# Performance work log

Measured on AMD Instinct MI355X. Metric: run time of the kernel, lower is better.

Reference implementation:

```python
import jax, jax.numpy as jnp
import numpy as np


def setup_inputs() -> dict:
    key = jax.random.key(0)
    B, C, H, W = 64, 128, 64, 64
    x = jax.random.normal(key, (B, C, H, W), dtype=jnp.float32)
    return {"x": x}


def reference(x) -> jnp.ndarray:
    # Covariance pooling: y = x_flat @ I_hat @ x_flat^T with
    # I_hat = (1/M) I - (1/M^2) ones(M,M).
    # Algebraically identical to (1/M) * (x - mean)(x - mean)^T, which
    # avoids materializing the MxM centering matrix.
    B, C, H, W = x.shape
    M = H * W
    xf = x.reshape(B, C, M)
    xc = xf - jnp.mean(xf, axis=2, keepdims=True)  # center over spatial dim
    y = jnp.einsum('bcm,bdm->bcd', xc, xc) / M     # [B, C, C]
    return y
```

## Files before the change

kernel.cpp:

```cpp
#include <hip/hip_runtime.h>
#include <hip/hip_bf16.h>

typedef __bf16 bf16x8 __attribute__((ext_vector_type(8)));
typedef float  f32x4  __attribute__((ext_vector_type(4)));

#define B_      64
#define C_      128
#define M_      4096
#define KCHUNK  4
#define KC      (M_ / KCHUNK)
#define BK      64
#define NSLAB   (KC / BK)
#define LSTR    72

__device__ __forceinline__ unsigned short f2bf(float f) {
  unsigned u = __builtin_bit_cast(unsigned, f);
  u += 0x7fffu + ((u >> 16) & 1u);
  return (unsigned short)(u >> 16);
}

__global__ __launch_bounds__(256) void covpool_main(
    const float* __restrict__ x, float* __restrict__ Gp, float* __restrict__ Sp) {
  __shared__ unsigned short As[2][C_ * LSTR];

  const int tid = threadIdx.x;
  const int b   = blockIdx.x >> 2;
  const int ch  = blockIdx.x & 3;

  const int r  = tid >> 2;
  const int c4 = (tid & 3) << 4;

  const float* xp0 = x + ((size_t)(b * C_ + r) * M_) + (size_t)ch * KC + c4;
  const float* xp1 = xp0 + (size_t)64 * M_;

  const int lane = tid & 63;
  const int wave = tid >> 6;
  const int row0 = (wave >> 1) << 6;
  const int col0 = (wave & 1) << 6;
  const int lrow = lane & 15;
  const int quad = lane >> 4;

  f32x4 acc[4][4];
#pragma unroll
  for (int i = 0; i < 4; ++i)
#pragma unroll
    for (int j = 0; j < 4; ++j)
      acc[i][j] = (f32x4){0.f, 0.f, 0.f, 0.f};

  float sum0 = 0.f, sum1 = 0.f;

  float4 regs[2][8];
#pragma unroll
  for (int q = 0; q < 4; ++q) {
    regs[0][q]     = ((const float4*)xp0)[q];
    regs[0][4 + q] = ((const float4*)xp1)[q];
  }

  for (int s = 0; s < NSLAB; ++s) {
    const int cur = s & 1;
    if (s + 1 < NSLAB) {
      const float4* p0 = (const float4*)(xp0 + (size_t)(s + 1) * BK);
      const float4* p1 = (const float4*)(xp1 + (size_t)(s + 1) * BK);
#pragma unroll
      for (int q = 0; q < 4; ++q) {
        regs[cur ^ 1][q]     = p0[q];
        regs[cur ^ 1][4 + q] = p1[q];
      }
    }
    unsigned short* d0 = &As[cur][r * LSTR + c4];
    unsigned short* d1 = &As[cur][(64 + r) * LSTR + c4];
#pragma unroll
    for (int q = 0; q < 4; ++q) {
      float4 v = regs[cur][q];
      sum0 += (v.x + v.y) + (v.z + v.w);
      ushort4 pk0 = { f2bf(v.x), f2bf(v.y), f2bf(v.z), f2bf(v.w) };
      *(ushort4*)(d0 + q * 4) = pk0;
      float4 w = regs[cur][4 + q];
      sum1 += (w.x + w.y) + (w.z + w.w);
      ushort4 pk1 = { f2bf(w.x), f2bf(w.y), f2bf(w.z), f2bf(w.w) };
      *(ushort4*)(d1 + q * 4) = pk1;
    }
    __syncthreads();

#pragma unroll
    for (int ks = 0; ks < 2; ++ks) {
      const int koff = ks * 32 + quad * 8;
      bf16x8 af[4], bfr[4];
#pragma unroll
      for (int i = 0; i < 4; ++i)
        af[i] = *(const bf16x8*)&As[cur][(row0 + i * 16 + lrow) * LSTR + koff];
#pragma unroll
      for (int j = 0; j < 4; ++j)
        bfr[j] = *(const bf16x8*)&As[cur][(col0 + j * 16 + lrow) * LSTR + koff];
#pragma unroll
      for (int i = 0; i < 4; ++i)
#pragma unroll
        for (int j = 0; j < 4; ++j)
          acc[i][j] = __builtin_amdgcn_mfma_f32_16x16x32_bf16(af[i], bfr[j], acc[i][j], 0, 0, 0);
    }
    __syncthreads();
  }

  float* gout = Gp + (((size_t)ch * B_ + b) << 14);
#pragma unroll
  for (int i = 0; i < 4; ++i)
#pragma unroll
    for (int j = 0; j < 4; ++j)
#pragma unroll
      for (int rr = 0; rr < 4; ++rr)
        gout[(size_t)(row0 + i * 16 + quad * 4 + rr) * C_ + (col0 + j * 16 + lrow)] = acc[i][j][rr];

  sum0 += __shfl_xor(sum0, 1); sum0 += __shfl_xor(sum0, 2);
  sum1 += __shfl_xor(sum1, 1); sum1 += __shfl_xor(sum1, 2);
  if ((tid & 3) == 0) {
    float* sout = Sp + (((size_t)ch * B_ + b) << 7);
    sout[r]      = sum0;
    sout[64 + r] = sum1;
  }
}

__global__ __launch_bounds__(256) void covpool_fix(
    const float* __restrict__ Gp, const float* __restrict__ Sp, float* __restrict__ y) {
  const int idx = blockIdx.x * 256 + threadIdx.x;
  const int bb  = idx >> 14;
  const int rem = idx & 16383;
  const int cc  = rem >> 7;
  const int dd  = rem & 127;
  float g = 0.f, sc = 0.f, sd = 0.f;
#pragma unroll
  for (int ch = 0; ch < KCHUNK; ++ch) {
    g  += Gp[(((size_t)ch * B_ + bb) << 14) + rem];
    sc += Sp[(((size_t)ch * B_ + bb) << 7) + cc];
    sd += Sp[(((size_t)ch * B_ + bb) << 7) + dd];
  }
  const float invM = 1.f / (float)M_;
  y[idx] = g * invM - (sc * invM) * (sd * invM);
}

extern "C" void kernel_launch(void* const* d_in, const int* in_sizes, int n_in,
                              void* d_out, int out_size, void* d_ws, size_t ws_size,
                              hipStream_t stream) {
  const float* x = (const float*)d_in[0];
  float* out = (float*)d_out;
  float* wsG = (float*)d_ws;
  float* wsS = wsG + (size_t)KCHUNK * B_ * C_ * C_;
  covpool_main<<<dim3(B_ * KCHUNK), dim3(256), 0, stream>>>(x, wsG, wsS);
  covpool_fix<<<dim3((B_ * C_ * C_) / 256), dim3(256), 0, stream>>>(wsG, wsS, out);
}
```

Before: 229.8 us.

## Split K into 8 chunks, use 512-thread blocks, store bf16 partial Gram matrices

Doubles the K split so 512 blocks cover the GPU instead of 256. Blocks grow to 512 threads (8 waves, each computing a 64x32 tile), and the slab loop is manually unrolled into an explicit double buffer. Partial Gram sums are written as bf16 to halve workspace traffic, and the reduction kernel is vectorized to handle four outputs per thread. Rounding the partials to bf16 adds precision error on top of the bf16 inputs, which could threaten tolerance, especially after the mean subtraction.

Result: faster. 195.9 us (-14.7%).

```diff
diff --git a/kernel.cpp b/kernel.cpp
--- a/kernel.cpp
+++ b/kernel.cpp
@@ -1,13 +1,13 @@
 #include <hip/hip_runtime.h>
-#include <hip/hip_bf16.h>
 
 typedef __bf16 bf16x8 __attribute__((ext_vector_type(8)));
 typedef float  f32x4  __attribute__((ext_vector_type(4)));
+typedef unsigned short us8 __attribute__((ext_vector_type(8)));
 
 #define B_      64
 #define C_      128
 #define M_      4096
-#define KCHUNK  4
+#define KCHUNK  8
 #define KC      (M_ / KCHUNK)
 #define BK      64
 #define NSLAB   (KC / BK)
@@ -18,123 +18,143 @@
   u += 0x7fffu + ((u >> 16) & 1u);
   return (unsigned short)(u >> 16);
 }
+__device__ __forceinline__ float bf2f(unsigned short h) {
+  unsigned u = ((unsigned)h) << 16;
+  return __builtin_bit_cast(float, u);
+}
 
-__global__ __launch_bounds__(256) void covpool_main(
-    const float* __restrict__ x, float* __restrict__ Gp, float* __restrict__ Sp) {
+__global__ __launch_bounds__(512, 4) void covpool_main(
+    const float* __restrict__ x, unsigned short* __restrict__ Gp, float* __restrict__ Sp) {
   __shared__ unsigned short As[2][C_ * LSTR];
 
-  const int tid = threadIdx.x;
-  const int b   = blockIdx.x >> 2;
-  const int ch  = blockIdx.x & 3;
+  const int tid  = threadIdx.x;
+  const int b    = blockIdx.x >> 3;
+  const int ch   = blockIdx.x & 7;
 
-  const int r  = tid >> 2;
-  const int c4 = (tid & 3) << 4;
+  const int row  = tid >> 3;
+  const int col8 = tid & 7;
 
-  const float* xp0 = x + ((size_t)(b * C_ + r) * M_) + (size_t)ch * KC + c4;
+  const float* xp0 = x + ((size_t)(b * C_ + row) * M_) + (size_t)ch * KC + col8 * 8;
   const float* xp1 = xp0 + (size_t)64 * M_;
 
   const int lane = tid & 63;
   const int wave = tid >> 6;
-  const int row0 = (wave >> 1) << 6;
-  const int col0 = (wave & 1) << 6;
+  const int row0 = (wave >> 2) << 6;
+  const int col0 = (wave & 3) << 5;
   const int lrow = lane & 15;
   const int quad = lane >> 4;
 
-  f32x4 acc[4][4];
+  f32x4 acc[4][2];
 #pragma unroll
   for (int i = 0; i < 4; ++i)
 #pragma unroll
-    for (int j = 0; j < 4; ++j)
+    for (int j = 0; j < 2; ++j)
       acc[i][j] = (f32x4){0.f, 0.f, 0.f, 0.f};
 
   float sum0 = 0.f, sum1 = 0.f;
 
-  float4 regs[2][8];
-#pragma unroll
-  for (int q = 0; q < 4; ++q) {
-    regs[0][q]     = ((const float4*)xp0)[q];
-    regs[0][4 + q] = ((const float4*)xp1)[q];
+  float4 a0, a1, a2, a3, b0, b1, b2, b3;
+
+  a0 = ((const float4*)xp0)[0]; a1 = ((const float4*)xp0)[1];
+  a2 = ((const float4*)xp1)[0]; a3 = ((const float4*)xp1)[1];
+
+#define STAGE(BUF, R0, R1, R2, R3)                                                  \
+  {                                                                                 \
+    sum0 += (R0.x + R0.y) + (R0.z + R0.w) + (R1.x + R1.y) + (R1.z + R1.w);          \
+    sum1 += (R2.x + R2.y) + (R2.z + R2.w) + (R3.x + R3.y) + (R3.z + R3.w);          \
+    us8 v0 = { f2bf(R0.x), f2bf(R0.y), f2bf(R0.z), f2bf(R0.w),                      \
+               f2bf(R1.x), f2bf(R1.y), f2bf(R1.z), f2bf(R1.w) };                    \
+    us8 v1 = { f2bf(R2.x), f2bf(R2.y), f2bf(R2.z), f2bf(R2.w),                      \
+               f2bf(R3.x), f2bf(R3.y), f2bf(R3.z), f2bf(R3.w) };                    \
+    *(__shared__ us8*)&As[BUF][row * LSTR + col8 * 8]        = v0;                  \
+    *(__shared__ us8*)&As[BUF][(64 + row) * LSTR + col8 * 8] = v1;                  \
   }
 
-  for (int s = 0; s < NSLAB; ++s) {
-    const int cur = s & 1;
-    if (s + 1 < NSLAB) {
-      const float4* p0 = (const float4*)(xp0 + (size_t)(s + 1) * BK);
-      const float4* p1 = (const float4*)(xp1 + (size_t)(s + 1) * BK);
-#pragma unroll
-      for (int q = 0; q < 4; ++q) {
-        regs[cur ^ 1][q]     = p0[q];
-        regs[cur ^ 1][4 + q] = p1[q];
-      }
-    }
-    unsigned short* d0 = &As[cur][r * LSTR + c4];
-    unsigned short* d1 = &As[cur][(64 + r) * LSTR + c4];
-#pragma unroll
-    for (int q = 0; q < 4; ++q) {
-      float4 v = regs[cur][q];
-      sum0 += (v.x + v.y) + (v.z + v.w);
-      ushort4 pk0 = { f2bf(v.x), f2bf(v.y), f2bf(v.z), f2bf(v.w) };
-      *(ushort4*)(d0 + q * 4) = pk0;
-      float4 w = regs[cur][4 + q];
-      sum1 += (w.x + w.y) + (w.z + w.w);
-      ushort4 pk1 = { f2bf(w.x), f2bf(w.y), f2bf(w.z), f2bf(w.w) };
-      *(ushort4*)(d1 + q * 4) = pk1;
-    }
-    __syncthreads();
+#define COMPUTE(BUF)                                                                \
+  {                                                                                 \
+    _Pragma("unroll")                                                               \
+    for (int ks = 0; ks < 2; ++ks) {                                                \
+      const int koff = ks * 32 + quad * 8;                                          \
+      bf16x8 af[4], bfr[2];                                                         \
+      _Pragma("unroll")                                                             \
+      for (int i = 0; i < 4; ++i)                                                   \
+        af[i] = *(const __shared__ bf16x8*)&As[BUF][(row0 + i * 16 + lrow) * LSTR + koff]; \
+      _Pragma("unroll")                                                             \
+      for (int j = 0; j < 2; ++j)                                                   \
+        bfr[j] = *(const __shared__ bf16x8*)&As[BUF][(col0 + j * 16 + lrow) * LSTR + koff]; \
+      _Pragma("unroll")                                                             \
+      for (int i = 0; i < 4; ++i)                                                   \
+        _Pragma("unroll")                                                           \
+        for (int j = 0; j < 2; ++j)                                                 \
+          acc[i][j] = __builtin_amdgcn_mfma_f32_16x16x32_bf16(af[i], bfr[j], acc[i][j], 0, 0, 0); \
+    }                                                                               \
+  }
 
 #pragma unroll
-    for (int ks = 0; ks < 2; ++ks) {
-      const int koff = ks * 32 + quad * 8;
-      bf16x8 af[4], bfr[4];
-#pragma unroll
-      for (int i = 0; i < 4; ++i)
-        af[i] = *(const bf16x8*)&As[cur][(row0 + i * 16 + lrow) * LSTR + koff];
-#pragma unroll
-      for (int j = 0; j < 4; ++j)
-        bfr[j] = *(const bf16x8*)&As[cur][(col0 + j * 16 + lrow) * LSTR + koff];
-#pragma unroll
-      for (int i = 0; i < 4; ++i)
-#pragma unroll
-        for (int j = 0; j < 4; ++j)
-          acc[i][j] = __builtin_amdgcn_mfma_f32_16x16x32_bf16(af[i], bfr[j], acc[i][j], 0, 0, 0);
+  for (int s = 0; s < NSLAB; s += 2) {
+    {
+      const float* p0 = xp0 + (size_t)(s + 1) * BK;
+      const float* p1 = xp1 + (size_t)(s + 1) * BK;
+      b0 = ((const float4*)p0)[0]; b1 = ((const float4*)p0)[1];
+      b2 = ((const float4*)p1)[0]; b3 = ((const float4*)p1)[1];
     }
+    STAGE(0, a0, a1, a2, a3);
     __syncthreads();
+    COMPUTE(0);
+    if (s + 2 < NSLAB) {
+      const float* p0 = xp0 + (size_t)(s + 2) * BK;
+      const float* p1 = xp1 + (size_t)(s + 2) * BK;
+      a0 = ((const float4*)p0)[0]; a1 = ((const float4*)p0)[1];
+      a2 = ((const float4*)p1)[0]; a3 = ((const float4*)p1)[1];
+    }
+    STAGE(1, b0, b1, b2, b3);
+    __syncthreads();
+    COMPUTE(1);
   }
 
-  float* gout = Gp + (((size_t)ch * B_ + b) << 14);
+  unsigned short* gout = Gp + (((size_t)ch * B_ + b) << 14);
 #pragma unroll
   for (int i = 0; i < 4; ++i)
 #pragma unroll
-    for (int j = 0; j < 4; ++j)
+    for (int j = 0; j < 2; ++j)
 #pragma unroll
       for (int rr = 0; rr < 4; ++rr)
-        gout[(size_t)(row0 + i * 16 + quad * 4 + rr) * C_ + (col0 + j * 16 + lrow)] = acc[i][j][rr];
+        gout[(size_t)(row0 + i * 16 + quad * 4 + rr) * C_ + (col0 + j * 16 + lrow)] =
+            f2bf(acc[i][j][rr]);
 
-  sum0 += __shfl_xor(sum0, 1); sum0 += __shfl_xor(sum0, 2);
-  sum1 += __shfl_xor(sum1, 1); sum1 += __shfl_xor(sum1, 2);
-  if ((tid & 3) == 0) {
+  sum0 += __shfl_xor(sum0, 1); sum0 += __shfl_xor(sum0, 2); sum0 += __shfl_xor(sum0, 4);
+  sum1 += __shfl_xor(sum1, 1); sum1 += __shfl_xor(sum1, 2); sum1 += __shfl_xor(sum1, 4);
+  if ((tid & 7) == 0) {
     float* sout = Sp + (((size_t)ch * B_ + b) << 7);
-    sout[r]      = sum0;
-    sout[64 + r] = sum1;
+    sout[row]      = sum0;
+    sout[64 + row] = sum1;
   }
 }
 
 __global__ __launch_bounds__(256) void covpool_fix(
-    const float* __restrict__ Gp, const float* __restrict__ Sp, float* __restrict__ y) {
-  const int idx = blockIdx.x * 256 + threadIdx.x;
+    const unsigned short* __restrict__ Gp, const float* __restrict__ Sp,
+    float* __restrict__ y) {
+  const int idx = (blockIdx.x * 256 + threadIdx.x) * 4;
   const int bb  = idx >> 14;
   const int rem = idx & 16383;
   const int cc  = rem >> 7;
   const int dd  = rem & 127;
-  float g = 0.f, sc = 0.f, sd = 0.f;
+  float g0 = 0.f, g1 = 0.f, g2 = 0.f, g3 = 0.f, sc = 0.f;
+  float4 sd = {0.f, 0.f, 0.f, 0.f};
 #pragma unroll
   for (int ch = 0; ch < KCHUNK; ++ch) {
-    g  += Gp[(((size_t)ch * B_ + bb) << 14) + rem];
-    sc += Sp[(((size_t)ch * B_ + bb) << 7) + cc];
-    sd += Sp[(((size_t)ch * B_ + bb) << 7) + dd];
+    ushort4 gv = *(const ushort4*)&Gp[(((size_t)ch * B_ + bb) << 14) + rem];
+    g0 += bf2f(gv.x); g1 += bf2f(gv.y); g2 += bf2f(gv.z); g3 += bf2f(gv.w);
+    const float* sp = Sp + (((size_t)ch * B_ + bb) << 7);
+    sc += sp[cc];
+    float4 s4 = *(const float4*)&sp[dd];
+    sd.x += s4.x; sd.y += s4.y; sd.z += s4.z; sd.w += s4.w;
   }
   const float invM = 1.f / (float)M_;
-  y[idx] = g * invM - (sc * invM) * (sd * invM);
+  const float scm = sc * invM;
+  float4 out = { g0 * invM - scm * (sd.x * invM), g1 * invM - scm * (sd.y * invM),
+                 g2 * invM - scm * (sd.z * invM), g3 * invM - scm * (sd.w * invM) };
+  *(float4*)&y[idx] = out;
 }
 
 extern "C" void kernel_launch(void* const* d_in, const int* in_sizes, int n_in,
@@ -142,8 +162,8 @@
                               hipStream_t stream) {
   const float* x = (const float*)d_in[0];
   float* out = (float*)d_out;
-  float* wsG = (float*)d_ws;
-  float* wsS = wsG + (size_t)KCHUNK * B_ * C_ * C_;
-  covpool_main<<<dim3(B_ * KCHUNK), dim3(256), 0, stream>>>(x, wsG, wsS);
-  covpool_fix<<<dim3((B_ * C_ * C_) / 256), dim3(256), 0, stream>>>(wsG, wsS, out);
+  unsigned short* wsG = (unsigned short*)d_ws;
+  float* wsS = (float*)(wsG + (size_t)KCHUNK * B_ * C_ * C_);
+  covpool_main<<<dim3(B_ * KCHUNK), dim3(512), 0, stream>>>(x, wsG, wsS);
+  covpool_fix<<<dim3((B_ * C_ * C_) / 1024), dim3(256), 0, stream>>>(wsG, wsS, out);
 }
```
